# Kernel optimization log

Hardware: AMD Instinct MI355X
Metric: run time of the kernel (lower is better)

Reference implementation:

```python
import jax, jax.numpy as jnp
import numpy as np

B, C, H, W = 4, 256, 64, 64
HID = C // 2


def setup_inputs() -> dict:
    key = jax.random.key(0)
    kx, kp, kt, kg, km = jax.random.split(key, 5)
    return {
        "x": jax.random.normal(kx, (B, C, H, W), dtype=jnp.float32),
        "w_phi": jax.random.normal(kp, (HID, C), dtype=jnp.float32) * 0.02,
        "w_theta": jax.random.normal(kt, (HID, C), dtype=jnp.float32) * 0.02,
        "w_g": jax.random.normal(kg, (HID, C), dtype=jnp.float32) * 0.02,
        "w_mask": jax.random.normal(km, (C, HID), dtype=jnp.float32) * 0.02,
    }


def reference(x, w_phi, w_theta, w_g, w_mask):
    b, c, h, w = x.shape
    n = h * w
    xf = x.reshape(b, c, n)                     # [B,C,N]
    # 1x1 convs == channel GEMMs
    phi = jnp.einsum('oc,bcn->bon', w_phi, xf)      # [B,HID,N]
    theta = jnp.einsum('oc,bcn->bon', w_theta, xf)  # [B,HID,N]
    g = jnp.einsum('oc,bcn->bon', w_g, xf)          # [B,HID,N]
    # attn[b,n,m] = sum_c theta[b,c,n] * phi[b,c,m]   (theta^T @ phi)
    attn = jnp.einsum('bcn,bcm->bnm', theta, phi)   # [B,N,N]
    # Faithful to nn.Softmax(dim=1): normalize over axis 1 (theta index)
    attn = jax.nn.softmax(attn, axis=1)
    # attn_g[b,n,c] = sum_m attn[b,n,m] * g[b,c,m]   (attn @ g^T)
    attn_g = jnp.einsum('bnm,bcm->bcn', attn, g)    # [B,HID,N] (already transposed back)
    mask = jnp.einsum('oc,bcn->bon', w_mask, attn_g).reshape(b, c, h, w)
    return mask + x
```

## Files before the change

kernel.cpp:

```cpp
#include <hip/hip_runtime.h>


#define NB   4
#define CIN  256
#define HIDN 128
#define NPIX 4096

typedef __attribute__((ext_vector_type(8))) short short8;
typedef __attribute__((ext_vector_type(4))) float f32x4;
typedef __attribute__((ext_vector_type(16))) float f32x16;

__device__ __forceinline__ unsigned short f2bf(float f) {
    unsigned u = __builtin_bit_cast(unsigned, f);
    u += 0x7fffu + ((u >> 16) & 1u);
    return (unsigned short)(u >> 16);
}
__device__ __forceinline__ unsigned f2bf2(float lo, float hi) {
    return (unsigned)f2bf(lo) | ((unsigned)f2bf(hi) << 16);
}
__device__ __forceinline__ float bf2f(unsigned short s) {
    return __builtin_bit_cast(float, (unsigned)s << 16);
}
__device__ __forceinline__ void cp16(void* lds, const void* g) {
    __builtin_amdgcn_global_load_lds(
        (const __attribute__((address_space(1))) unsigned int*)g,
        (__attribute__((address_space(3))) unsigned int*)lds, 16, 0, 0);
}

__global__ __launch_bounds__(256) void k_prep_w(
    const float* __restrict__ wp, const float* __restrict__ wt,
    const float* __restrict__ wg, const float* __restrict__ wm,
    unsigned short* __restrict__ Wp, unsigned short* __restrict__ Wt,
    unsigned short* __restrict__ Wg, unsigned short* __restrict__ Wm)
{
    const int which = blockIdx.x >> 3;
    const float* src = (which == 0) ? wp : (which == 1) ? wt : (which == 2) ? wg : wm;
    unsigned short* dst = (which == 0) ? Wp : (which == 1) ? Wt : (which == 2) ? Wg : Wm;
#pragma unroll
    for (int t = 0; t < 2; ++t) {
        const int gidx = ((blockIdx.x & 7) * 256 + threadIdx.x) * 2 + t;
        int o, srcc, dstc;
        if (which < 3) {
            o = gidx >> 5;
            const int gc = gidx & 31;
            const int sg = (gc & ~15) | ((gc & 15) ^ (o & 15));
            srcc = o * 256 + gc * 8; dstc = o * 256 + sg * 8;
        } else {
            o = gidx >> 4;
            const int gc = gidx & 15;
            const int sg = gc ^ (o & 15);
            srcc = o * 128 + gc * 8; dstc = o * 128 + sg * 8;
        }
        float4 a = *(const float4*)&src[srcc];
        float4 b = *(const float4*)&src[srcc + 4];
        uint4 v;
        v.x = f2bf2(a.x, a.y); v.y = f2bf2(a.z, a.w);
        v.z = f2bf2(b.x, b.y); v.w = f2bf2(b.z, b.w);
        *(uint4*)&dst[dstc] = v;
    }
}

__global__ __launch_bounds__(256) void k_prep_x(
    const float* __restrict__ x,
    unsigned short* __restrict__ xT,
    float* __restrict__ colsum)
{
    const int nt = blockIdx.x, ct = blockIdx.y, b = blockIdx.z;
    const int tid = threadIdx.x;
    if (ct == 0 && tid < 64) colsum[(size_t)b * NPIX + nt * 64 + tid] = 0.f;

    __shared__ unsigned short Ls[64][66];
    {
        const int c_loc = tid >> 2, n_seg = (tid & 3) * 16;
        const float* src = x + ((size_t)(b * CIN + ct * 64 + c_loc)) * NPIX + nt * 64 + n_seg;
#pragma unroll
        for (int j = 0; j < 8; ++j)
            *(unsigned*)&Ls[c_loc][n_seg + 2 * j] = f2bf2(src[2 * j], src[2 * j + 1]);
    }
    __syncthreads();
    {
        const int n_loc = tid >> 2, c_seg = (tid & 3) * 16;
        const int n_glob = nt * 64 + n_loc;
        unsigned short tmp[16];
#pragma unroll
        for (int j = 0; j < 16; ++j) tmp[j] = Ls[c_seg + j][n_loc];
#pragma unroll
        for (int gr = 0; gr < 2; ++gr) {
            const int c_base = ct * 64 + c_seg + gr * 8;
            const int sec = c_base >> 7;
            const int sg = (((c_base >> 3) & 15) ^ (n_glob & 15));
            *(uint4*)&xT[((size_t)b * NPIX + n_glob) * CIN + sec * 128 + sg * 8] =
                *(uint4*)&tmp[gr * 8];
        }
    }
}

__global__ __launch_bounds__(256, 3) void k_proj(
    const unsigned short* __restrict__ Wp,
    const unsigned short* __restrict__ Wt,
    const unsigned short* __restrict__ Wg,
    const unsigned short* __restrict__ xT,
    unsigned short* __restrict__ phiT,
    unsigned short* __restrict__ thetaT,
    unsigned short* __restrict__ gbuf)
{
    const int nt = blockIdx.x, ot = blockIdx.y, b = blockIdx.z;
    const unsigned short* W = (ot == 0) ? Wp : (ot == 1) ? Wt : Wg;

    __shared__ alignas(16) unsigned short Aw[128][128];
    __shared__ alignas(16) unsigned short Bx[64][128];

    const int tid = threadIdx.x;
    const int wave = tid >> 6, lane = tid & 63;
    const int oh = wave >> 1, nh = wave & 1;
    const int l31 = lane & 31, lh = lane >> 5;
    const int key = l31 & 15;

    f32x16 acc[2];
#pragma unroll
    for (int r = 0; r < 16; ++r) { acc[0][r] = 0.f; acc[1][r] = 0.f; }

    for (int kh = 0; kh < 2; ++kh) {
        __syncthreads();
#pragma unroll
        for (int i = 0; i < 8; ++i) {
            const int u = i * 256 + tid;
            cp16(&Aw[0][0] + u * 8, W + (u >> 4) * 256 + kh * 128 + (u & 15) * 8);
        }
#pragma unroll
        for (int i = 0; i < 4; ++i) {
            const int u = i * 256 + tid;
            cp16(&Bx[0][0] + u * 8,
                 xT + ((size_t)b * NPIX + nt * 64 + (u >> 4)) * CIN + kh * 128 + (u & 15) * 8);
        }
        __syncthreads();
#pragma unroll
        for (int ks = 0; ks < 8; ++ks) {
            const int g = ((ks * 2 + lh) ^ key) << 3;
            short8 bb = *(const short8*)&Bx[nh * 32 + l31][g];
#pragma unroll
            for (int t = 0; t < 2; ++t) {
                short8 a = *(const short8*)&Aw[oh * 64 + t * 32 + l31][g];
                acc[t] = __builtin_amdgcn_mfma_f32_32x32x16_bf16(a, bb, acc[t], 0, 0, 0);
            }
        }
    }

    const int n_glob = nt * 64 + nh * 32 + l31;
    if (ot < 2) {
        unsigned short* T = (ot == 0) ? phiT : thetaT;
#pragma unroll
        for (int t = 0; t < 2; ++t)
#pragma unroll
            for (int rg = 0; rg < 4; ++rg) {
                const int ob = oh * 64 + t * 32 + 8 * rg + 4 * lh;
                const int sc = (((ob >> 3) ^ (n_glob & 15)) << 3) | (ob & 7);
                uint2 v;
                v.x = f2bf2(acc[t][rg * 4 + 0], acc[t][rg * 4 + 1]);
                v.y = f2bf2(acc[t][rg * 4 + 2], acc[t][rg * 4 + 3]);
                *(uint2*)&T[((size_t)b * NPIX + n_glob) * HIDN + sc] = v;
            }
    } else {
        const int sbase = n_glob & ~127;
        const int g16 = (n_glob >> 3) & 15, c7off = n_glob & 7;
#pragma unroll
        for (int t = 0; t < 2; ++t)
#pragma unroll
            for (int r = 0; r < 16; ++r) {
                const int c = oh * 64 + t * 32 + (r & 3) + 8 * (r >> 2) + 4 * lh;
                const int sc = sbase | ((g16 ^ (c & 15)) << 3) | c7off;
                gbuf[((size_t)b * HIDN + c) * NPIX + sc] = f2bf(acc[t][r]);
            }
    }
}

__global__ __launch_bounds__(256, 3) void k_colsum(
    const unsigned short* __restrict__ thetaT,
    const unsigned short* __restrict__ phiT,
    float* __restrict__ colsum,
    float* __restrict__ O32)
{
    const int mt = blockIdx.x, ng = blockIdx.y, b = blockIdx.z;
    const int tid = threadIdx.x;
    {
        const int blin = ((blockIdx.z * 8 + blockIdx.y) * 32 + blockIdx.x);
        float* p = O32 + (size_t)blin * 2048 + tid * 8;
        *(f32x4*)p = f32x4{0.f, 0.f, 0.f, 0.f};
        *(f32x4*)(p + 4) = f32x4{0.f, 0.f, 0.f, 0.f};
    }

    __shared__ alignas(16) unsigned short As[64][128];

    const int wave = tid >> 6, lane = tid & 63;
    const int wn = wave & 1, wh = wave >> 1;
    const int l31 = lane & 31, lh = lane >> 5;
    const int key = l31 & 15;

    short8 bfrag[2][8];
#pragma unroll
    for (int t = 0; t < 2; ++t) {
        const int m = mt * 128 + wn * 64 + t * 32 + l31;
        const unsigned short* src = phiT + ((size_t)b * NPIX + m) * HIDN;
#pragma unroll
        for (int ks = 0; ks < 8; ++ks)
            bfrag[t][ks] = *(const short8*)(src + (((ks * 2 + lh) ^ key) << 3));
    }

    float csum[2] = {0.f, 0.f};

    for (int nc = 0; nc < 8; ++nc) {
        const int n0 = ng * 512 + nc * 64;
        __syncthreads();
#pragma unroll
        for (int i = 0; i < 4; ++i) {
            const int u = i * 256 + tid;
            cp16(&As[0][0] + u * 8,
                 thetaT + ((size_t)b * NPIX + n0 + (u >> 4)) * HIDN + (u & 15) * 8);
        }
        __syncthreads();

        f32x16 acc[2];
#pragma unroll
        for (int r = 0; r < 16; ++r) { acc[0][r] = 0.f; acc[1][r] = 0.f; }
#pragma unroll
        for (int ks = 0; ks < 8; ++ks) {
            short8 a = *(const short8*)&As[wh * 32 + l31][(((ks * 2 + lh) ^ key) << 3)];
            acc[0] = __builtin_amdgcn_mfma_f32_32x32x16_bf16(a, bfrag[0][ks], acc[0], 0, 0, 0);
            acc[1] = __builtin_amdgcn_mfma_f32_32x32x16_bf16(a, bfrag[1][ks], acc[1], 0, 0, 0);
        }
#pragma unroll
        for (int t = 0; t < 2; ++t)
#pragma unroll
            for (int r = 0; r < 16; ++r) csum[t] += __expf(acc[t][r]);
    }

#pragma unroll
    for (int t = 0; t < 2; ++t) {
        float s = csum[t];
        s += __shfl_xor(s, 32);
        if (lh == 0)
            atomicAdd(&colsum[(size_t)b * NPIX + mt * 128 + wn * 64 + t * 32 + l31], s);
    }
}

__global__ __launch_bounds__(256) void k_scale_g(
    unsigned short* __restrict__ gbuf, const float* __restrict__ colsum)
{
    const int idx = blockIdx.x * 256 + threadIdx.x;
    const int row = idx >> 9;
    const int sc = (idx & 511) * 8;
    const int bb = row >> 7;
    const int mt = (sc & ~127) | ((((sc >> 3) & 15) ^ (row & 15)) << 3);
    uint4 v = *(uint4*)&gbuf[(size_t)row * NPIX + sc];
    float4 c0 = *(const float4*)&colsum[(size_t)bb * NPIX + mt];
    float4 c1 = *(const float4*)&colsum[(size_t)bb * NPIX + mt + 4];
    unsigned short* vs = (unsigned short*)&v;
    const float cs[8] = {c0.x, c0.y, c0.z, c0.w, c1.x, c1.y, c1.z, c1.w};
#pragma unroll
    for (int j = 0; j < 8; ++j) vs[j] = f2bf(bf2f(vs[j]) / cs[j]);
    *(uint4*)&gbuf[(size_t)row * NPIX + sc] = v;
}

__global__ __launch_bounds__(256, 2) void k_attn(
    const unsigned short* __restrict__ thetaT,
    const unsigned short* __restrict__ phiT,
    const unsigned short* __restrict__ gbuf,
    float* __restrict__ O32)
{
    const int nt = blockIdx.x, ms = blockIdx.y, b = blockIdx.z;
    const int n0 = nt * 64;

    __shared__ alignas(16) unsigned short Ts[64][128];
    __shared__ alignas(16) unsigned short Gs[128][128];
    __shared__ alignas(16) unsigned short Ps[64][136];

    const int tid = threadIdx.x;
    const int wave = tid >> 6, lane = tid & 63;
    const int q = wave;
    const int nh = wave >> 1, ch = wave & 1;
    const int l31 = lane & 31, lh = lane >> 5;
    const int key = l31 & 15;

#pragma unroll
    for (int i = 0; i < 4; ++i) {
        const int u = i * 256 + tid;
        cp16(&Ts[0][0] + u * 8,
             thetaT + ((size_t)b * NPIX + n0 + (u >> 4)) * HIDN + (u & 15) * 8);
    }

    short8 pcur[8], pnxt[8];
    {
        const unsigned short* src = phiT + ((size_t)b * NPIX + ms * 2048 + q * 32 + l31) * HIDN;
#pragma unroll
        for (int ks = 0; ks < 8; ++ks)
            pcur[ks] = *(const short8*)(src + (((ks * 2 + lh) ^ key) << 3));
    }

    f32x16 accO[2];
#pragma unroll
    for (int r = 0; r < 16; ++r) { accO[0][r] = 0.f; accO[1][r] = 0.f; }

    __syncthreads();

    for (int mc = 0; mc < 16; ++mc) {
        const int m0 = ms * 2048 + mc * 128;
#pragma unroll
        for (int i = 0; i < 8; ++i) {
            const int u = i * 256 + tid;
            cp16(&Gs[0][0] + u * 8,
                 gbuf + ((size_t)b * HIDN + (u >> 4)) * NPIX + m0 + (u & 15) * 8);
        }
        if (mc < 15) {
            const unsigned short* src =
                phiT + ((size_t)b * NPIX + m0 + 128 + q * 32 + l31) * HIDN;
#pragma unroll
            for (int ks = 0; ks < 8; ++ks)
                pnxt[ks] = *(const short8*)(src + (((ks * 2 + lh) ^ key) << 3));
        }

        f32x16 accS[2];
#pragma unroll
        for (int r = 0; r < 16; ++r) { accS[0][r] = 0.f; accS[1][r] = 0.f; }
#pragma unroll
        for (int ks = 0; ks < 8; ++ks) {
            const int g = ((ks * 2 + lh) ^ key) << 3;
            short8 t0 = *(const short8*)&Ts[l31][g];
            short8 t1 = *(const short8*)&Ts[32 + l31][g];
            accS[0] = __builtin_amdgcn_mfma_f32_32x32x16_bf16(pcur[ks], t0, accS[0], 0, 0, 0);
            accS[1] = __builtin_amdgcn_mfma_f32_32x32x16_bf16(pcur[ks], t1, accS[1], 0, 0, 0);
        }
#pragma unroll
        for (int t = 0; t < 2; ++t) {
            const int n = t * 32 + l31;
#pragma unroll
            for (int rg = 0; rg < 4; ++rg) {
                uint2 v;
                v.x = f2bf2(__expf(accS[t][rg * 4 + 0]), __expf(accS[t][rg * 4 + 1]));
                v.y = f2bf2(__expf(accS[t][rg * 4 + 2]), __expf(accS[t][rg * 4 + 3]));
                const int gm = q * 4 + rg;
                const int col = (((gm ^ (n & 15)) << 3) | (4 * lh));
                *(uint2*)&Ps[n][col] = v;
            }
        }
        __syncthreads();

#pragma unroll
        for (int ks = 0; ks < 8; ++ks) {
            const int g = ((ks * 2 + lh) ^ key) << 3;
            short8 pa = *(const short8*)&Ps[nh * 32 + l31][g];
            short8 g0 = *(const short8*)&Gs[ch * 64 + l31][g];
            short8 g1 = *(const short8*)&Gs[ch * 64 + 32 + l31][g];
            accO[0] = __builtin_amdgcn_mfma_f32_32x32x16_bf16(pa, g0, accO[0], 0, 0, 0);
            accO[1] = __builtin_amdgcn_mfma_f32_32x32x16_bf16(pa, g1, accO[1], 0, 0, 0);
        }
        __syncthreads();

#pragma unroll
        for (int ks = 0; ks < 8; ++ks) pcur[ks] = pnxt[ks];
    }

#pragma unroll
    for (int t = 0; t < 2; ++t)
#pragma unroll
        for (int r = 0; r < 16; ++r) {
            const int n = n0 + nh * 32 + (r & 3) + 8 * (r >> 2) + 4 * lh;
            const int c = ch * 64 + t * 32 + l31;
            atomicAdd(&O32[((size_t)b * NPIX + n) * HIDN + c], accO[t][r]);
        }
}

__global__ __launch_bounds__(256, 3) void k_mask(
    const unsigned short* __restrict__ Wm,
    const float* __restrict__ O32,
    const float* __restrict__ x,
    float* __restrict__ out)
{
    const int nt = blockIdx.x, ct = blockIdx.y, b = blockIdx.z;
    __shared__ alignas(16) unsigned short As[128][128];
    __shared__ alignas(16) unsigned short Bs[64][128];

    const int tid = threadIdx.x;
    const int wave = tid >> 6, lane = tid & 63;
    const int oh = wave >> 1, nh = wave & 1;
    const int l31 = lane & 31, lh = lane >> 5;
    const int key = l31 & 15;

#pragma unroll
    for (int i = 0; i < 8; ++i) {
        const int u = i * 256 + tid;
        cp16(&As[0][0] + u * 8, Wm + (ct * 128 + (u >> 4)) * HIDN + (u & 15) * 8);
    }
    {
        const int n_loc = tid >> 2, seg = (tid & 3) * 32;
        const float* src = O32 + ((size_t)b * NPIX + nt * 64 + n_loc) * HIDN + seg;
        const int k7 = n_loc & 7;
#pragma unroll
        for (int j = 0; j < 4; ++j) {
            const int gr = (seg >> 3) + j;
            const int sg = (gr & ~7) | ((gr & 7) ^ k7);
            const float* s8 = src + j * 8;
            unsigned* d = (unsigned*)&Bs[n_loc][sg * 8];
#pragma unroll
            for (int k = 0; k < 4; ++k) d[k] = f2bf2(s8[2 * k], s8[2 * k + 1]);
        }
    }
    __syncthreads();

    f32x16 acc[2];
#pragma unroll
    for (int r = 0; r < 16; ++r) { acc[0][r] = 0.f; acc[1][r] = 0.f; }
#pragma unroll
    for (int ks = 0; ks < 8; ++ks) {
        const int gr = ks * 2 + lh;
        const int sgb = ((gr & ~7) | ((gr & 7) ^ (l31 & 7))) << 3;
        short8 bb = *(const short8*)&Bs[nh * 32 + l31][sgb];
#pragma unroll
        for (int t = 0; t < 2; ++t) {
            short8 a = *(const short8*)&As[oh * 64 + t * 32 + l31][((gr ^ key) << 3)];
            acc[t] = __builtin_amdgcn_mfma_f32_32x32x16_bf16(a, bb, acc[t], 0, 0, 0);
        }
    }

    const int n = nt * 64 + nh * 32 + l31;
#pragma unroll
    for (int t = 0; t < 2; ++t)
#pragma unroll
        for (int r = 0; r < 16; ++r) {
            const int co = ct * 128 + oh * 64 + t * 32 + (r & 3) + 8 * (r >> 2) + 4 * lh;
            const size_t idx = ((size_t)b * CIN + co) * NPIX + n;
            out[idx] = acc[t][r] + x[idx];
        }
}

extern "C" void kernel_launch(void* const* d_in, const int* in_sizes, int n_in,
                              void* d_out, int out_size, void* d_ws, size_t ws_size,
                              hipStream_t stream)
{
    (void)in_sizes; (void)n_in; (void)out_size; (void)ws_size;
    const float* x       = (const float*)d_in[0];
    const float* w_phi   = (const float*)d_in[1];
    const float* w_theta = (const float*)d_in[2];
    const float* w_g     = (const float*)d_in[3];
    const float* w_mask  = (const float*)d_in[4];
    float* out = (float*)d_out;

    char* ws = (char*)d_ws;
    unsigned short* phiT   = (unsigned short*)(ws);
    unsigned short* thetaT = (unsigned short*)(ws + 4194304);
    unsigned short* gbuf   = (unsigned short*)(ws + 8388608);
    float*          colsum = (float*)(ws + 12582912);
    unsigned short* xT     = (unsigned short*)(ws + 12648448);
    float*          O32    = (float*)(ws + 12648448);
    unsigned short* Wp     = (unsigned short*)(ws + 21037056);
    unsigned short* Wt     = (unsigned short*)(ws + 21102592);
    unsigned short* Wg     = (unsigned short*)(ws + 21168128);
    unsigned short* Wm     = (unsigned short*)(ws + 21233664);

    k_prep_w <<<dim3(32),        256, 0, stream>>>(w_phi, w_theta, w_g, w_mask, Wp, Wt, Wg, Wm);
    k_prep_x <<<dim3(64, 4, 4),  256, 0, stream>>>(x, xT, colsum);
    k_proj   <<<dim3(64, 3, 4),  256, 0, stream>>>(Wp, Wt, Wg, xT, phiT, thetaT, gbuf);
    k_colsum <<<dim3(32, 8, 4),  256, 0, stream>>>(thetaT, phiT, colsum, O32);
    k_scale_g<<<dim3(1024),      256, 0, stream>>>(gbuf, colsum);
    k_attn   <<<dim3(64, 2, 4),  256, 0, stream>>>(thetaT, phiT, gbuf, O32);
    k_mask   <<<dim3(64, 2, 4),  256, 0, stream>>>(Wm, O32, x, out);
}
```

Before: 193.9 us.

## Double-buffer theta and G tiles and keep theta fragments in registers

In k_colsum the theta tile is now double-buffered in LDS, so the next chunk loads while MFMAs run on the current one, and one barrier per iteration is removed. In k_attn the G tile is double-buffered in LDS and its next chunk is prefetched right after the P barrier. Theta fragments are loaded once into registers instead of staged in LDS, and the now-unneeded Ps row padding is dropped. The change hides global-load latency behind compute, at the cost of more LDS per block (about 80KB) and roughly 64 extra VGPRs for theta fragments, which may hurt occupancy.

```diff
diff --git a/kernel.cpp b/kernel.cpp
--- a/kernel.cpp
+++ b/kernel.cpp
@@ -189,7 +189,7 @@
         *(f32x4*)(p + 4) = f32x4{0.f, 0.f, 0.f, 0.f};
     }
 
-    __shared__ alignas(16) unsigned short As[64][128];
+    __shared__ alignas(16) unsigned short As[2][64][128];
 
     const int wave = tid >> 6, lane = tid & 63;
     const int wn = wave & 1, wh = wave >> 1;
@@ -206,25 +206,34 @@
             bfrag[t][ks] = *(const short8*)(src + (((ks * 2 + lh) ^ key) << 3));
     }
 
+#pragma unroll
+    for (int i = 0; i < 4; ++i) {
+        const int u = i * 256 + tid;
+        cp16(&As[0][0][0] + u * 8,
+             thetaT + ((size_t)b * NPIX + ng * 512 + (u >> 4)) * HIDN + (u & 15) * 8);
+    }
+
     float csum[2] = {0.f, 0.f};
 
     for (int nc = 0; nc < 8; ++nc) {
-        const int n0 = ng * 512 + nc * 64;
+        const int cur = nc & 1;
         __syncthreads();
-#pragma unroll
-        for (int i = 0; i < 4; ++i) {
-            const int u = i * 256 + tid;
-            cp16(&As[0][0] + u * 8,
-                 thetaT + ((size_t)b * NPIX + n0 + (u >> 4)) * HIDN + (u & 15) * 8);
-        }
-        __syncthreads();
+        if (nc < 7) {
+            const int n1 = ng * 512 + (nc + 1) * 64;
+#pragma unroll
+            for (int i = 0; i < 4; ++i) {
+                const int u = i * 256 + tid;
+                cp16(&As[cur ^ 1][0][0] + u * 8,
+                     thetaT + ((size_t)b * NPIX + n1 + (u >> 4)) * HIDN + (u & 15) * 8);
+            }
+        }
 
         f32x16 acc[2];
 #pragma unroll
         for (int r = 0; r < 16; ++r) { acc[0][r] = 0.f; acc[1][r] = 0.f; }
 #pragma unroll
         for (int ks = 0; ks < 8; ++ks) {
-            short8 a = *(const short8*)&As[wh * 32 + l31][(((ks * 2 + lh) ^ key) << 3)];
+            short8 a = *(const short8*)&As[cur][wh * 32 + l31][(((ks * 2 + lh) ^ key) << 3)];
             acc[0] = __builtin_amdgcn_mfma_f32_32x32x16_bf16(a, bfrag[0][ks], acc[0], 0, 0, 0);
             acc[1] = __builtin_amdgcn_mfma_f32_32x32x16_bf16(a, bfrag[1][ks], acc[1], 0, 0, 0);
         }
@@ -270,9 +279,8 @@
     const int nt = blockIdx.x, ms = blockIdx.y, b = blockIdx.z;
     const int n0 = nt * 64;
 
-    __shared__ alignas(16) unsigned short Ts[64][128];
-    __shared__ alignas(16) unsigned short Gs[128][128];
-    __shared__ alignas(16) unsigned short Ps[64][136];
+    __shared__ alignas(16) unsigned short Gs[2][128][128];
+    __shared__ alignas(16) unsigned short Ps[64][128];
 
     const int tid = threadIdx.x;
     const int wave = tid >> 6, lane = tid & 63;
@@ -281,34 +289,45 @@
     const int l31 = lane & 31, lh = lane >> 5;
     const int key = l31 & 15;
 
-#pragma unroll
-    for (int i = 0; i < 4; ++i) {
-        const int u = i * 256 + tid;
-        cp16(&Ts[0][0] + u * 8,
-             thetaT + ((size_t)b * NPIX + n0 + (u >> 4)) * HIDN + (u & 15) * 8);
-    }
-
+    short8 tfrag[2][8];
+#pragma unroll
+    for (int t = 0; t < 2; ++t) {
+        const unsigned short* src =
+            thetaT + ((size_t)b * NPIX + n0 + t * 32 + l31) * HIDN;
+#pragma unroll
+        for (int ks = 0; ks < 8; ++ks)
+            tfrag[t][ks] = *(const short8*)(src + (((ks * 2 + lh) ^ key) << 3));
+    }
     short8 pcur[8], pnxt[8];
     {
-        const unsigned short* src = phiT + ((size_t)b * NPIX + ms * 2048 + q * 32 + l31) * HIDN;
+        const unsigned short* src =
+            phiT + ((size_t)b * NPIX + ms * 2048 + q * 32 + l31) * HIDN;
 #pragma unroll
         for (int ks = 0; ks < 8; ++ks)
             pcur[ks] = *(const short8*)(src + (((ks * 2 + lh) ^ key) << 3));
     }
+#pragma unroll
+    for (int i = 0; i < 8; ++i) {
+        const int u = i * 256 + tid;
+        cp16(&Gs[0][0][0] + u * 8,
+             gbuf + ((size_t)b * HIDN + (u >> 4)) * NPIX + ms * 2048 + (u & 15) * 8);
+    }
 
     f32x16 accO[2];
 #pragma unroll
     for (int r = 0; r < 16; ++r) { accO[0][r] = 0.f; accO[1][r] = 0.f; }
 
-    __syncthreads();
-
     for (int mc = 0; mc < 16; ++mc) {
+        const int cur = mc & 1;
         const int m0 = ms * 2048 + mc * 128;
-#pragma unroll
-        for (int i = 0; i < 8; ++i) {
-            const int u = i * 256 + tid;
-            cp16(&Gs[0][0] + u * 8,
-                 gbuf + ((size_t)b * HIDN + (u >> 4)) * NPIX + m0 + (u & 15) * 8);
+
+        f32x16 accS[2];
+#pragma unroll
+        for (int r = 0; r < 16; ++r) { accS[0][r] = 0.f; accS[1][r] = 0.f; }
+#pragma unroll
+        for (int ks = 0; ks < 8; ++ks) {
+            accS[0] = __builtin_amdgcn_mfma_f32_32x32x16_bf16(pcur[ks], tfrag[0][ks], accS[0], 0, 0, 0);
+            accS[1] = __builtin_amdgcn_mfma_f32_32x32x16_bf16(pcur[ks], tfrag[1][ks], accS[1], 0, 0, 0);
         }
         if (mc < 15) {
             const unsigned short* src =
@@ -316,18 +335,6 @@
 #pragma unroll
             for (int ks = 0; ks < 8; ++ks)
                 pnxt[ks] = *(const short8*)(src + (((ks * 2 + lh) ^ key) << 3));
-        }
-
-        f32x16 accS[2];
-#pragma unroll
-        for (int r = 0; r < 16; ++r) { accS[0][r] = 0.f; accS[1][r] = 0.f; }
-#pragma unroll
-        for (int ks = 0; ks < 8; ++ks) {
-            const int g = ((ks * 2 + lh) ^ key) << 3;
-            short8 t0 = *(const short8*)&Ts[l31][g];
-            short8 t1 = *(const short8*)&Ts[32 + l31][g];
-            accS[0] = __builtin_amdgcn_mfma_f32_32x32x16_bf16(pcur[ks], t0, accS[0], 0, 0, 0);
-            accS[1] = __builtin_amdgcn_mfma_f32_32x32x16_bf16(pcur[ks], t1, accS[1], 0, 0, 0);
         }
 #pragma unroll
         for (int t = 0; t < 2; ++t) {
@@ -338,18 +345,25 @@
                 v.x = f2bf2(__expf(accS[t][rg * 4 + 0]), __expf(accS[t][rg * 4 + 1]));
                 v.y = f2bf2(__expf(accS[t][rg * 4 + 2]), __expf(accS[t][rg * 4 + 3]));
                 const int gm = q * 4 + rg;
-                const int col = (((gm ^ (n & 15)) << 3) | (4 * lh));
+                const int col = ((gm ^ (n & 15)) << 3) | (4 * lh);
                 *(uint2*)&Ps[n][col] = v;
             }
         }
         __syncthreads();
-
+        if (mc < 15) {
+#pragma unroll
+            for (int i = 0; i < 8; ++i) {
+                const int u = i * 256 + tid;
+                cp16(&Gs[cur ^ 1][0][0] + u * 8,
+                     gbuf + ((size_t)b * HIDN + (u >> 4)) * NPIX + m0 + 128 + (u & 15) * 8);
+            }
+        }
 #pragma unroll
         for (int ks = 0; ks < 8; ++ks) {
             const int g = ((ks * 2 + lh) ^ key) << 3;
             short8 pa = *(const short8*)&Ps[nh * 32 + l31][g];
-            short8 g0 = *(const short8*)&Gs[ch * 64 + l31][g];
-            short8 g1 = *(const short8*)&Gs[ch * 64 + 32 + l31][g];
+            short8 g0 = *(const short8*)&Gs[cur][ch * 64 + l31][g];
+            short8 g1 = *(const short8*)&Gs[cur][ch * 64 + 32 + l31][g];
             accO[0] = __builtin_amdgcn_mfma_f32_32x32x16_bf16(pa, g0, accO[0], 0, 0, 0);
             accO[1] = __builtin_amdgcn_mfma_f32_32x32x16_bf16(pa, g1, accO[1], 0, 0, 0);
         }
```

After: 169.5 us. 1.14x faster.
